# Kernel tuning notes

Measured on AMD Instinct MI355X. Metric: run time of the kernel, lower is better.

The kernel has to match this reference:

```python
import jax, jax.numpy as jnp
import numpy as np

N = 100000
E = 1600000
IN_DIM, HID, OUT = 128, 64, 32
SLOPE = 0.1


def setup_inputs() -> dict:
    key = jax.random.key(0)
    ks = jax.random.split(key, 8)
    x = jax.random.normal(ks[0], (N, IN_DIM), dtype=jnp.float32)
    edge_index = jax.random.randint(ks[1], (2, E), 0, N, dtype=jnp.int64)
    s1 = 1.0 / np.sqrt(IN_DIM)
    s2 = 1.0 / np.sqrt(HID)
    W_l1 = jax.random.uniform(ks[2], (IN_DIM, HID), jnp.float32, -s1, s1)
    W_r1 = jax.random.uniform(ks[3], (IN_DIM, HID), jnp.float32, -s1, s1)
    b1 = jax.random.uniform(ks[4], (HID,), jnp.float32, -s1, s1)
    W_l2 = jax.random.uniform(ks[5], (HID, OUT), jnp.float32, -s2, s2)
    W_r2 = jax.random.uniform(ks[6], (HID, OUT), jnp.float32, -s2, s2)
    b2 = jax.random.uniform(ks[7], (OUT,), jnp.float32, -s2, s2)
    return {"x": x, "edge_index": edge_index,
            "W_l1": W_l1, "W_r1": W_r1, "b1": b1,
            "W_l2": W_l2, "W_r2": W_r2, "b2": b2}


def _sage_conv(h, src, dst, deg_inv, W_l, W_r, b):
    # mean-aggregate neighbor features: gather from src, scatter-add to dst
    agg = jax.ops.segment_sum(h[src], dst, num_segments=N) * deg_inv  # [N, d]
    return agg @ W_l + h @ W_r + b


def reference(x, edge_index, W_l1, W_r1, b1, W_l2, W_r2, b2):
    src, dst = edge_index[0], edge_index[1]
    deg = jax.ops.segment_sum(jnp.ones((E,), x.dtype), dst, num_segments=N)
    deg_inv = (1.0 / jnp.maximum(deg, 1.0))[:, None]  # [N, 1]
    h = jax.nn.leaky_relu(_sage_conv(x, src, dst, deg_inv, W_l1, W_r1, b1), SLOPE)
    z = jax.nn.leaky_relu(_sage_conv(h, src, dst, deg_inv, W_l2, W_r2, b2), SLOPE)
    return z
```

## Files before the change

### kernel.cpp

```cpp
#include <hip/hip_runtime.h>


constexpr int IN_DIM  = 128;
constexpr int HID     = 64;
constexpr int OUT_DIM = 32;
constexpr float SLOPE = 0.1f;
constexpr int NPB_SHIFT = 8;
constexpr int NBMAX = 512;
constexpr int CHUNK = 4096;

typedef unsigned int uint32;
typedef unsigned short ushort16;

__device__ inline float blo(uint32 u) { return __uint_as_float(u << 16); }
__device__ inline float bhi(uint32 u) { return __uint_as_float(u & 0xffff0000u); }
__device__ inline ushort16 f2b(float f) {
    uint32 u = __float_as_uint(f);
    u += 0x7fffu + ((u >> 16) & 1u);
    return (ushort16)(u >> 16);
}
__device__ inline uint32 pack2(float lo, float hi) {
    return (uint32)f2b(lo) | ((uint32)f2b(hi) << 16);
}
__device__ inline void addup(float* acc, uint4 u) {
    acc[0] += blo(u.x); acc[1] += bhi(u.x);
    acc[2] += blo(u.y); acc[3] += bhi(u.y);
    acc[4] += blo(u.z); acc[5] += bhi(u.z);
    acc[6] += blo(u.w); acc[7] += bhi(u.w);
}

__global__ __launch_bounds__(256) void bucket_hist_kernel(
    const int* __restrict__ dst, int* __restrict__ bhist, int E) {
    __shared__ int bh[NBMAX];
    for (int i = threadIdx.x; i < NBMAX; i += 256) bh[i] = 0;
    __syncthreads();
    for (int e = blockIdx.x * 256 + threadIdx.x; e < E; e += gridDim.x * 256)
        atomicAdd(&bh[dst[e] >> NPB_SHIFT], 1);
    __syncthreads();
    for (int b = threadIdx.x; b < NBMAX; b += 256)
        if (bh[b]) atomicAdd(&bhist[b], bh[b]);
}

__global__ __launch_bounds__(512) void bucket_scan_kernel(
    const int* __restrict__ bhist, int* __restrict__ ebase,
    int* __restrict__ pbase, int* __restrict__ bcur,
    int* __restrict__ rowptr, int NB, int N, int E) {
    __shared__ int s1[512], s2[512];
    const int t = threadIdx.x;
    int bh = (t < NB) ? bhist[t] : 0;
    int pd = (bh + 15) & ~15;
    s1[t] = bh; s2[t] = pd; __syncthreads();
    for (int off = 1; off < 512; off <<= 1) {
        int a = (t >= off) ? s1[t - off] : 0;
        int b = (t >= off) ? s2[t - off] : 0;
        __syncthreads();
        s1[t] += a; s2[t] += b;
        __syncthreads();
    }
    ebase[t] = s1[t] - bh;
    pbase[t] = s2[t] - pd;
    bcur[t]  = s2[t] - pd;
    if (t == 0) rowptr[N] = E;
}

__global__ __launch_bounds__(256) void partition_kernel(
    const int* __restrict__ src, const int* __restrict__ dst,
    int* __restrict__ bcur, uint32* __restrict__ pairs, int E, int NB) {
    __shared__ int hist[NBMAX], loff[NBMAX], cur[NBMAX];
    __shared__ int s[256];
    __shared__ uint32 stage[CHUNK];
    const int tid = threadIdx.x;
    const int e0  = blockIdx.x * CHUNK;
    const int cnt = min(CHUNK, E - e0);
    for (int i = tid; i < NBMAX; i += 256) hist[i] = 0;
    __syncthreads();
    int sreg[16], dreg[16];
#pragma unroll
    for (int k = 0; k < 16; ++k) {
        int i = tid + k * 256;
        if (i < cnt) {
            sreg[k] = src[e0 + i];
            dreg[k] = dst[e0 + i];
            atomicAdd(&hist[dreg[k] >> NPB_SHIFT], 1);
        }
    }
    __syncthreads();
    int a0 = hist[2 * tid], a1 = hist[2 * tid + 1];
    s[tid] = a0 + a1; __syncthreads();
    for (int off = 1; off < 256; off <<= 1) {
        int t = (tid >= off) ? s[tid - off] : 0;
        __syncthreads();
        s[tid] += t;
        __syncthreads();
    }
    int ex = s[tid] - (a0 + a1);
    loff[2 * tid] = ex;      loff[2 * tid + 1] = ex + a0;
    cur[2 * tid]  = ex;      cur[2 * tid + 1]  = ex + a0;
    __syncthreads();
#pragma unroll
    for (int k = 0; k < 16; ++k) {
        int i = tid + k * 256;
        if (i < cnt) {
            int b = dreg[k] >> NPB_SHIFT;
            int pos = atomicAdd(&cur[b], 1);
            stage[pos] = (uint32)sreg[k] | ((uint32)(dreg[k] & 255) << 24);
        }
    }
    __syncthreads();
    for (int b = tid; b < NB; b += 256) {
        int cb = hist[b];
        if (cb) {
            int g  = atomicAdd(&bcur[b], cb);
            int lb = loff[b];
            for (int k = 0; k < cb; ++k) pairs[g + k] = stage[lb + k];
        }
    }
}

__global__ __launch_bounds__(256) void fine_bin_kernel(
    const uint32* __restrict__ pairs, const int* __restrict__ bhist,
    const int* __restrict__ ebase, const int* __restrict__ pbase,
    int* __restrict__ rowptr, int* __restrict__ srcs, int N) {
    __shared__ int h2[256], cur[256], s[256];
    const int tid  = threadIdx.x;
    const int b    = blockIdx.x;
    const int n0   = b << NPB_SHIFT;
    const int base = pbase[b];
    const int sz   = bhist[b];
    h2[tid] = 0;
    __syncthreads();
    for (int i = tid; i < sz; i += 256)
        atomicAdd(&h2[pairs[base + i] >> 24], 1);
    __syncthreads();
    int v = h2[tid]; s[tid] = v; __syncthreads();
    for (int off = 1; off < 256; off <<= 1) {
        int t = (tid >= off) ? s[tid - off] : 0;
        __syncthreads();
        s[tid] += t;
        __syncthreads();
    }
    int rp = ebase[b] + s[tid] - v;
    int n  = n0 + tid;
    if (n < N) rowptr[n] = rp;
    cur[tid] = rp;
    __syncthreads();
    for (int i = tid; i < sz; i += 256) {
        uint32 u = pairs[base + i];
        int p = atomicAdd(&cur[u >> 24], 1);
        srcs[p] = (int)(u & 0xFFFFFFu);
    }
}

__global__ __launch_bounds__(256) void gemm1_mfma_kernel(
    const float* __restrict__ x, const float* __restrict__ Wl,
    const float* __restrict__ Wr, const float* __restrict__ b1,
    ushort16* __restrict__ xl, float* __restrict__ xr, int N) {
    using frag = __attribute__((ext_vector_type(8))) short;
    using f32x4 = __attribute__((ext_vector_type(4))) float;
    constexpr int LDA = IN_DIM + 8;
    __shared__ ushort16 Ash[64][LDA];
    __shared__ ushort16 Bsh[128][LDA];
    const int tid = threadIdx.x;
    const int n0  = blockIdx.x * 64;
    {
        const int c = tid & 63;
        for (int k = tid >> 6; k < IN_DIM; k += 4) {
            Bsh[c][k]      = f2b(Wl[k * HID + c]);
            Bsh[c + 64][k] = f2b(Wr[k * HID + c]);
        }
    }
    {
        const int lc  = (tid & 31) * 4;
        for (int row = tid >> 5; row < 64; row += 8) {
            int node = n0 + row;
            float4 xv = (node < N)
                ? *reinterpret_cast<const float4*>(&x[(long)node * IN_DIM + lc])
                : float4{0.f, 0.f, 0.f, 0.f};
            ushort16 pk[4] = {f2b(xv.x), f2b(xv.y), f2b(xv.z), f2b(xv.w)};
            *reinterpret_cast<ushort2*>(&Ash[row][lc])     = ushort2{pk[0], pk[1]};
            *reinterpret_cast<ushort2*>(&Ash[row][lc + 2]) = ushort2{pk[2], pk[3]};
        }
    }
    __syncthreads();
    const int lane = tid & 63;
    const int m0   = (tid >> 6) * 16;
    const int mlo  = lane & 15;
    const int qk   = lane >> 4;
    frag Af[4];
#pragma unroll
    for (int kc = 0; kc < 4; ++kc)
        Af[kc] = *reinterpret_cast<const frag*>(&Ash[m0 + mlo][kc * 32 + qk * 8]);
#pragma unroll
    for (int ct = 0; ct < 8; ++ct) {
        f32x4 acc = {0.f, 0.f, 0.f, 0.f};
#pragma unroll
        for (int kc = 0; kc < 4; ++kc) {
            frag Bf = *reinterpret_cast<const frag*>(&Bsh[ct * 16 + mlo][kc * 32 + qk * 8]);
            acc = __builtin_amdgcn_mfma_f32_16x16x32_bf16(Af[kc], Bf, acc, 0, 0, 0);
        }
        const int col = ct * 16 + mlo;
#pragma unroll
        for (int r = 0; r < 4; ++r) {
            int node = n0 + m0 + qk * 4 + r;
            if (node < N) {
                if (col < HID) xl[(long)node * HID + col] = f2b(acc[r]);
                else           xr[(long)node * HID + (col - HID)] = acc[r] + b1[col - HID];
            }
        }
    }
}

__global__ __launch_bounds__(256) void agg1_kernel(
    const int* __restrict__ rowptr, const int* __restrict__ srcs,
    const uint4* __restrict__ xlq,
    const float* __restrict__ xr,
    uint4* __restrict__ hq, int N) {
    const int lane  = threadIdx.x & 63;
    const int li    = lane & 7;
    const int gbase = lane & 56;
    const int wave  = (blockIdx.x << 2) + (threadIdx.x >> 6);
    const int n     = wave * 8 + (lane >> 3);
    if (n >= N) return;
    const int rp = rowptr[n];
    const int d  = rowptr[n + 1] - rp;
    float acc[8] = {};
    int j = 0;
    while (j + 16 <= d) {
        int sA = srcs[rp + j + li];
        int sB = srcs[rp + j + 8 + li];
        uint4 u0[8], u1[8];
#pragma unroll
        for (int t = 0; t < 8; ++t) {
            int s = __shfl(sA, gbase + t);
            u0[t] = xlq[(long)s * 8 + li];
        }
#pragma unroll
        for (int t = 0; t < 8; ++t) {
            int s = __shfl(sB, gbase + t);
            u1[t] = xlq[(long)s * 8 + li];
        }
#pragma unroll
        for (int t = 0; t < 8; ++t) { addup(acc, u0[t]); addup(acc, u1[t]); }
        j += 16;
    }
    if (j + 8 <= d) {
        int sA = srcs[rp + j + li];
        uint4 u0[8];
#pragma unroll
        for (int t = 0; t < 8; ++t) {
            int s = __shfl(sA, gbase + t);
            u0[t] = xlq[(long)s * 8 + li];
        }
#pragma unroll
        for (int t = 0; t < 8; ++t) addup(acc, u0[t]);
        j += 8;
    }
    int r = d - j;
    if (r > 0) {
        int sA = srcs[rp + j + ((li < r) ? li : 0)];
#pragma unroll
        for (int t = 0; t < 7; ++t) {
            if (t < r) {
                int s = __shfl(sA, gbase + t);
                uint4 u = xlq[(long)s * 8 + li];
                addup(acc, u);
            }
        }
    }
    const float dinv = (d > 0) ? (1.f / (float)d) : 1.f;
    float4 xrA = *reinterpret_cast<const float4*>(&xr[(long)n * HID + 8 * li]);
    float4 xrB = *reinterpret_cast<const float4*>(&xr[(long)n * HID + 8 * li + 4]);
    float h[8];
    h[0] = fmaf(acc[0], dinv, xrA.x); h[1] = fmaf(acc[1], dinv, xrA.y);
    h[2] = fmaf(acc[2], dinv, xrA.z); h[3] = fmaf(acc[3], dinv, xrA.w);
    h[4] = fmaf(acc[4], dinv, xrB.x); h[5] = fmaf(acc[5], dinv, xrB.y);
    h[6] = fmaf(acc[6], dinv, xrB.z); h[7] = fmaf(acc[7], dinv, xrB.w);
#pragma unroll
    for (int t = 0; t < 8; ++t) h[t] = (h[t] > 0.f) ? h[t] : SLOPE * h[t];
    uint4 pk;
    pk.x = pack2(h[0], h[1]); pk.y = pack2(h[2], h[3]);
    pk.z = pack2(h[4], h[5]); pk.w = pack2(h[6], h[7]);
    hq[(long)n * 8 + li] = pk;
}

__global__ __launch_bounds__(256) void gemm2_mfma_kernel(
    const ushort16* __restrict__ hs, const float* __restrict__ Wl2,
    const float* __restrict__ Wr2, const float* __restrict__ b2,
    ushort16* __restrict__ hl, float* __restrict__ hr, int N) {
    using frag = __attribute__((ext_vector_type(8))) short;
    using f32x4 = __attribute__((ext_vector_type(4))) float;
    __shared__ ushort16 Bsh[64][72];
    const int tid = threadIdx.x;
    const int n0  = blockIdx.x * 64;
    {
        const int c = tid & 63;
        for (int k = tid >> 6; k < HID; k += 4) {
            float w = (c < OUT_DIM) ? Wl2[k * OUT_DIM + c]
                                    : Wr2[k * OUT_DIM + (c - OUT_DIM)];
            Bsh[c][k] = f2b(w);
        }
    }
    __syncthreads();
    const int lane = tid & 63;
    const int m0   = (tid >> 6) * 16;
    const int mlo  = lane & 15;
    const int qk   = lane >> 4;
    const int row  = n0 + m0 + mlo;
    const int arow = (row < N) ? row : 0;
    frag Af[2];
#pragma unroll
    for (int kc = 0; kc < 2; ++kc)
        Af[kc] = *reinterpret_cast<const frag*>(&hs[(long)arow * HID + kc * 32 + qk * 8]);
#pragma unroll
    for (int ct = 0; ct < 4; ++ct) {
        f32x4 acc = {0.f, 0.f, 0.f, 0.f};
#pragma unroll
        for (int kc = 0; kc < 2; ++kc) {
            frag Bf = *reinterpret_cast<const frag*>(&Bsh[ct * 16 + mlo][kc * 32 + qk * 8]);
            acc = __builtin_amdgcn_mfma_f32_16x16x32_bf16(Af[kc], Bf, acc, 0, 0, 0);
        }
        const int col = ct * 16 + mlo;
#pragma unroll
        for (int r = 0; r < 4; ++r) {
            int node = n0 + m0 + qk * 4 + r;
            if (node < N) {
                if (col < OUT_DIM) hl[(long)node * OUT_DIM + col] = f2b(acc[r]);
                else hr[(long)node * OUT_DIM + (col - OUT_DIM)] = acc[r] + b2[col - OUT_DIM];
            }
        }
    }
}

__global__ __launch_bounds__(256) void agg2_final_kernel(
    const int* __restrict__ rowptr, const int* __restrict__ srcs,
    const uint4* __restrict__ hlq,
    const float* __restrict__ hr,
    float* __restrict__ z, int N) {
    const int lane  = threadIdx.x & 63;
    const int li    = lane & 3;
    const int gbase = lane & 60;
    const int wave  = (blockIdx.x << 2) + (threadIdx.x >> 6);
    const int n     = wave * 16 + (lane >> 2);
    if (n >= N) return;
    const int rp = rowptr[n];
    const int d  = rowptr[n + 1] - rp;
    float acc[8] = {};
    int j = 0;
    while (j + 16 <= d) {
        int sA = srcs[rp + j + li];
        int sB = srcs[rp + j + 4 + li];
        int sC = srcs[rp + j + 8 + li];
        int sD = srcs[rp + j + 12 + li];
        uint4 u[16];
#pragma unroll
        for (int t = 0; t < 4; ++t) u[t]      = hlq[(long)__shfl(sA, gbase + t) * 4 + li];
#pragma unroll
        for (int t = 0; t < 4; ++t) u[4 + t]  = hlq[(long)__shfl(sB, gbase + t) * 4 + li];
#pragma unroll
        for (int t = 0; t < 4; ++t) u[8 + t]  = hlq[(long)__shfl(sC, gbase + t) * 4 + li];
#pragma unroll
        for (int t = 0; t < 4; ++t) u[12 + t] = hlq[(long)__shfl(sD, gbase + t) * 4 + li];
#pragma unroll
        for (int t = 0; t < 16; ++t) addup(acc, u[t]);
        j += 16;
    }
    while (j + 4 <= d) {
        int sA = srcs[rp + j + li];
        uint4 u[4];
#pragma unroll
        for (int t = 0; t < 4; ++t) u[t] = hlq[(long)__shfl(sA, gbase + t) * 4 + li];
#pragma unroll
        for (int t = 0; t < 4; ++t) addup(acc, u[t]);
        j += 4;
    }
    int r = d - j;
    if (r > 0) {
        int sA = srcs[rp + j + ((li < r) ? li : 0)];
#pragma unroll
        for (int t = 0; t < 3; ++t) {
            if (t < r) {
                uint4 u = hlq[(long)__shfl(sA, gbase + t) * 4 + li];
                addup(acc, u);
            }
        }
    }
    const float dinv = (d > 0) ? (1.f / (float)d) : 1.f;
    float4 hA = *reinterpret_cast<const float4*>(&hr[(long)n * OUT_DIM + 8 * li]);
    float4 hB = *reinterpret_cast<const float4*>(&hr[(long)n * OUT_DIM + 8 * li + 4]);
    float4 vA, vB;
    vA.x = fmaf(acc[0], dinv, hA.x); vA.y = fmaf(acc[1], dinv, hA.y);
    vA.z = fmaf(acc[2], dinv, hA.z); vA.w = fmaf(acc[3], dinv, hA.w);
    vB.x = fmaf(acc[4], dinv, hB.x); vB.y = fmaf(acc[5], dinv, hB.y);
    vB.z = fmaf(acc[6], dinv, hB.z); vB.w = fmaf(acc[7], dinv, hB.w);
    vA.x = (vA.x > 0.f) ? vA.x : SLOPE * vA.x;
    vA.y = (vA.y > 0.f) ? vA.y : SLOPE * vA.y;
    vA.z = (vA.z > 0.f) ? vA.z : SLOPE * vA.z;
    vA.w = (vA.w > 0.f) ? vA.w : SLOPE * vA.w;
    vB.x = (vB.x > 0.f) ? vB.x : SLOPE * vB.x;
    vB.y = (vB.y > 0.f) ? vB.y : SLOPE * vB.y;
    vB.z = (vB.z > 0.f) ? vB.z : SLOPE * vB.z;
    vB.w = (vB.w > 0.f) ? vB.w : SLOPE * vB.w;
    *reinterpret_cast<float4*>(&z[(long)n * OUT_DIM + 8 * li]) = vA;
    *reinterpret_cast<float4*>(&z[(long)n * OUT_DIM + 8 * li + 4]) = vB;
}

extern "C" void kernel_launch(void* const* d_in, const int* in_sizes, int n_in,
                              void* d_out, int out_size, void* d_ws, size_t ws_size,
                              hipStream_t stream) {
    const float* x   = (const float*)d_in[0];
    const int*   ei  = (const int*)d_in[1];
    const float* Wl1 = (const float*)d_in[2];
    const float* Wr1 = (const float*)d_in[3];
    const float* b1  = (const float*)d_in[4];
    const float* Wl2 = (const float*)d_in[5];
    const float* Wr2 = (const float*)d_in[6];
    const float* b2  = (const float*)d_in[7];

    const int N = in_sizes[0] / IN_DIM;
    const int E = in_sizes[1] / 2;
    const int* src = ei;
    const int* dst = ei + E;
    const int NB = (N + 255) >> NPB_SHIFT;

    char* p = (char*)d_ws;
    int* bhist    = (int*)p;           p += sizeof(int) * NBMAX;
    int* ebase    = (int*)p;           p += sizeof(int) * NBMAX;
    int* pbase    = (int*)p;           p += sizeof(int) * NBMAX;
    int* bcur     = (int*)p;           p += sizeof(int) * NBMAX;
    int* rowptr   = (int*)p;           p += sizeof(int) * (N + 4);
    uint32* pairs = (uint32*)p;        p += sizeof(uint32) * ((size_t)E + 16 * NBMAX);
    int* srcs     = (int*)p;           p += sizeof(int) * E;
    ushort16* xl  = (ushort16*)p;      p += sizeof(ushort16) * (size_t)N * HID;
    float* xr     = (float*)p;         p += sizeof(float) * (size_t)N * HID;
    ushort16* h   = (ushort16*)p;      p += sizeof(ushort16) * (size_t)N * HID;
    ushort16* hl  = (ushort16*)p;      p += sizeof(ushort16) * (size_t)N * OUT_DIM;
    float* hr     = (float*)p;         p += sizeof(float) * (size_t)N * OUT_DIM;

    hipMemsetAsync(bhist, 0, sizeof(int) * NBMAX, stream);

    bucket_hist_kernel<<<512, 256, 0, stream>>>(dst, bhist, E);
    bucket_scan_kernel<<<1, 512, 0, stream>>>(bhist, ebase, pbase, bcur, rowptr, NB, N, E);
    partition_kernel<<<(E + CHUNK - 1) / CHUNK, 256, 0, stream>>>(src, dst, bcur, pairs, E, NB);
    fine_bin_kernel<<<NB, 256, 0, stream>>>(pairs, bhist, ebase, pbase, rowptr, srcs, N);
    gemm1_mfma_kernel<<<(N + 63) / 64, 256, 0, stream>>>(x, Wl1, Wr1, b1, xl, xr, N);
    agg1_kernel<<<(N + 31) / 32, 256, 0, stream>>>(rowptr, srcs, (const uint4*)xl, xr,
                                                   (uint4*)h, N);
    gemm2_mfma_kernel<<<(N + 63) / 64, 256, 0, stream>>>(h, Wl2, Wr2, b2, hl, hr, N);
    agg2_final_kernel<<<(N + 63) / 64, 256, 0, stream>>>(rowptr, srcs, (const uint4*)hl, hr,
                                                         (float*)d_out, N);
}
```

Before: 279.1 us.

## Fuse CSR fine-binning into layer-1 aggregation and overlap histogram with GEMM1

Pre-converts weights to bf16 once in a prep kernel and drops the memset. Bucket histogramming now runs as extra blocks inside the GEMM1 launch so the two overlap. The fine-bin sort is merged into the layer-1 aggregation: each block sorts half a bucket's sources in LDS, then aggregates from LDS indices and writes rowptr, degree and srcs for layer 2. The partition write-back is also coalesced using a binary search over bucket offsets. This removes launches and global round-trips, at the cost of redundant per-half histogramming, two-node-per-wave passes, and a fixed LDS capacity (SUBCAP) per half-bucket.

```diff
diff --git a/kernel.cpp b/kernel.cpp
--- a/kernel.cpp
+++ b/kernel.cpp
@@ -8,6 +8,8 @@
 constexpr int NPB_SHIFT = 8;
 constexpr int NBMAX = 512;
 constexpr int CHUNK = 4096;
+constexpr int HIST_BLOCKS = 256;
+constexpr int SUBCAP = 4096;
 
 typedef unsigned int uint32;
 typedef unsigned short ushort16;
@@ -22,6 +24,7 @@
 __device__ inline uint32 pack2(float lo, float hi) {
     return (uint32)f2b(lo) | ((uint32)f2b(hi) << 16);
 }
+__device__ inline float lrelu(float v) { return (v > 0.f) ? v : SLOPE * v; }
 __device__ inline void addup(float* acc, uint4 u) {
     acc[0] += blo(u.x); acc[1] += bhi(u.x);
     acc[2] += blo(u.y); acc[3] += bhi(u.y);
@@ -29,148 +32,50 @@
     acc[6] += blo(u.w); acc[7] += bhi(u.w);
 }
 
-__global__ __launch_bounds__(256) void bucket_hist_kernel(
-    const int* __restrict__ dst, int* __restrict__ bhist, int E) {
-    __shared__ int bh[NBMAX];
-    for (int i = threadIdx.x; i < NBMAX; i += 256) bh[i] = 0;
-    __syncthreads();
-    for (int e = blockIdx.x * 256 + threadIdx.x; e < E; e += gridDim.x * 256)
-        atomicAdd(&bh[dst[e] >> NPB_SHIFT], 1);
-    __syncthreads();
-    for (int b = threadIdx.x; b < NBMAX; b += 256)
-        if (bh[b]) atomicAdd(&bhist[b], bh[b]);
-}
-
-__global__ __launch_bounds__(512) void bucket_scan_kernel(
-    const int* __restrict__ bhist, int* __restrict__ ebase,
-    int* __restrict__ pbase, int* __restrict__ bcur,
-    int* __restrict__ rowptr, int NB, int N, int E) {
-    __shared__ int s1[512], s2[512];
-    const int t = threadIdx.x;
-    int bh = (t < NB) ? bhist[t] : 0;
-    int pd = (bh + 15) & ~15;
-    s1[t] = bh; s2[t] = pd; __syncthreads();
-    for (int off = 1; off < 512; off <<= 1) {
-        int a = (t >= off) ? s1[t - off] : 0;
-        int b = (t >= off) ? s2[t - off] : 0;
-        __syncthreads();
-        s1[t] += a; s2[t] += b;
-        __syncthreads();
-    }
-    ebase[t] = s1[t] - bh;
-    pbase[t] = s2[t] - pd;
-    bcur[t]  = s2[t] - pd;
-    if (t == 0) rowptr[N] = E;
-}
-
-__global__ __launch_bounds__(256) void partition_kernel(
-    const int* __restrict__ src, const int* __restrict__ dst,
-    int* __restrict__ bcur, uint32* __restrict__ pairs, int E, int NB) {
-    __shared__ int hist[NBMAX], loff[NBMAX], cur[NBMAX];
-    __shared__ int s[256];
-    __shared__ uint32 stage[CHUNK];
-    const int tid = threadIdx.x;
-    const int e0  = blockIdx.x * CHUNK;
-    const int cnt = min(CHUNK, E - e0);
-    for (int i = tid; i < NBMAX; i += 256) hist[i] = 0;
-    __syncthreads();
-    int sreg[16], dreg[16];
-#pragma unroll
-    for (int k = 0; k < 16; ++k) {
-        int i = tid + k * 256;
-        if (i < cnt) {
-            sreg[k] = src[e0 + i];
-            dreg[k] = dst[e0 + i];
-            atomicAdd(&hist[dreg[k] >> NPB_SHIFT], 1);
-        }
-    }
-    __syncthreads();
-    int a0 = hist[2 * tid], a1 = hist[2 * tid + 1];
-    s[tid] = a0 + a1; __syncthreads();
-    for (int off = 1; off < 256; off <<= 1) {
-        int t = (tid >= off) ? s[tid - off] : 0;
-        __syncthreads();
-        s[tid] += t;
-        __syncthreads();
-    }
-    int ex = s[tid] - (a0 + a1);
-    loff[2 * tid] = ex;      loff[2 * tid + 1] = ex + a0;
-    cur[2 * tid]  = ex;      cur[2 * tid + 1]  = ex + a0;
-    __syncthreads();
-#pragma unroll
-    for (int k = 0; k < 16; ++k) {
-        int i = tid + k * 256;
-        if (i < cnt) {
-            int b = dreg[k] >> NPB_SHIFT;
-            int pos = atomicAdd(&cur[b], 1);
-            stage[pos] = (uint32)sreg[k] | ((uint32)(dreg[k] & 255) << 24);
-        }
-    }
-    __syncthreads();
-    for (int b = tid; b < NB; b += 256) {
-        int cb = hist[b];
-        if (cb) {
-            int g  = atomicAdd(&bcur[b], cb);
-            int lb = loff[b];
-            for (int k = 0; k < cb; ++k) pairs[g + k] = stage[lb + k];
-        }
-    }
-}
-
-__global__ __launch_bounds__(256) void fine_bin_kernel(
-    const uint32* __restrict__ pairs, const int* __restrict__ bhist,
-    const int* __restrict__ ebase, const int* __restrict__ pbase,
-    int* __restrict__ rowptr, int* __restrict__ srcs, int N) {
-    __shared__ int h2[256], cur[256], s[256];
-    const int tid  = threadIdx.x;
-    const int b    = blockIdx.x;
-    const int n0   = b << NPB_SHIFT;
-    const int base = pbase[b];
-    const int sz   = bhist[b];
-    h2[tid] = 0;
-    __syncthreads();
-    for (int i = tid; i < sz; i += 256)
-        atomicAdd(&h2[pairs[base + i] >> 24], 1);
-    __syncthreads();
-    int v = h2[tid]; s[tid] = v; __syncthreads();
-    for (int off = 1; off < 256; off <<= 1) {
-        int t = (tid >= off) ? s[tid - off] : 0;
-        __syncthreads();
-        s[tid] += t;
-        __syncthreads();
-    }
-    int rp = ebase[b] + s[tid] - v;
-    int n  = n0 + tid;
-    if (n < N) rowptr[n] = rp;
-    cur[tid] = rp;
-    __syncthreads();
-    for (int i = tid; i < sz; i += 256) {
-        uint32 u = pairs[base + i];
-        int p = atomicAdd(&cur[u >> 24], 1);
-        srcs[p] = (int)(u & 0xFFFFFFu);
-    }
-}
-
-__global__ __launch_bounds__(256) void gemm1_mfma_kernel(
-    const float* __restrict__ x, const float* __restrict__ Wl,
-    const float* __restrict__ Wr, const float* __restrict__ b1,
-    ushort16* __restrict__ xl, float* __restrict__ xr, int N) {
+__global__ __launch_bounds__(256) void prep_kernel(
+    const float* __restrict__ Wl1, const float* __restrict__ Wr1,
+    const float* __restrict__ Wl2, const float* __restrict__ Wr2,
+    ushort16* __restrict__ Wb1, ushort16* __restrict__ Wb2,
+    int* __restrict__ bhist) {
+    const int gid = blockIdx.x * 256 + threadIdx.x;
+    if (gid < NBMAX) bhist[gid] = 0;
+    for (int i = gid; i < 128 * 128; i += gridDim.x * 256) {
+        int c = i >> 7, k = i & 127;
+        Wb1[i] = f2b((c < HID) ? Wl1[k * HID + c] : Wr1[k * HID + (c - HID)]);
+    }
+    for (int i = gid; i < 64 * 64; i += gridDim.x * 256) {
+        int c = i >> 6, k = i & 63;
+        Wb2[i] = f2b((c < OUT_DIM) ? Wl2[k * OUT_DIM + c]
+                                   : Wr2[k * OUT_DIM + (c - OUT_DIM)]);
+    }
+}
+
+__global__ __launch_bounds__(256) void gemm1_hist_kernel(
+    const float* __restrict__ x, const ushort16* __restrict__ Wb1,
+    const float* __restrict__ b1,
+    const int* __restrict__ dst, int* __restrict__ bhist,
+    ushort16* __restrict__ xl, float* __restrict__ xr,
+    int N, int E, int ngemm) {
     using frag = __attribute__((ext_vector_type(8))) short;
     using f32x4 = __attribute__((ext_vector_type(4))) float;
     constexpr int LDA = IN_DIM + 8;
     __shared__ ushort16 Ash[64][LDA];
-    __shared__ ushort16 Bsh[128][LDA];
     const int tid = threadIdx.x;
-    const int n0  = blockIdx.x * 64;
+    if (blockIdx.x >= ngemm) {
+        int* bh = (int*)Ash;
+        for (int i = tid; i < NBMAX; i += 256) bh[i] = 0;
+        __syncthreads();
+        const int b0 = blockIdx.x - ngemm;
+        for (int e = b0 * 256 + tid; e < E; e += HIST_BLOCKS * 256)
+            atomicAdd(&bh[dst[e] >> NPB_SHIFT], 1);
+        __syncthreads();
+        for (int b = tid; b < NBMAX; b += 256)
+            if (bh[b]) atomicAdd(&bhist[b], bh[b]);
+        return;
+    }
+    const int n0 = blockIdx.x * 64;
     {
-        const int c = tid & 63;
-        for (int k = tid >> 6; k < IN_DIM; k += 4) {
-            Bsh[c][k]      = f2b(Wl[k * HID + c]);
-            Bsh[c + 64][k] = f2b(Wr[k * HID + c]);
-        }
-    }
-    {
-        const int lc  = (tid & 31) * 4;
+        const int lc = (tid & 31) * 4;
         for (int row = tid >> 5; row < 64; row += 8) {
             int node = n0 + row;
             float4 xv = (node < N)
@@ -195,7 +100,8 @@
         f32x4 acc = {0.f, 0.f, 0.f, 0.f};
 #pragma unroll
         for (int kc = 0; kc < 4; ++kc) {
-            frag Bf = *reinterpret_cast<const frag*>(&Bsh[ct * 16 + mlo][kc * 32 + qk * 8]);
+            frag Bf = *reinterpret_cast<const frag*>(
+                &Wb1[(ct * 16 + mlo) * 128 + kc * 32 + qk * 8]);
             acc = __builtin_amdgcn_mfma_f32_16x16x32_bf16(Af[kc], Bf, acc, 0, 0, 0);
         }
         const int col = ct * 16 + mlo;
@@ -210,97 +116,199 @@
     }
 }
 
-__global__ __launch_bounds__(256) void agg1_kernel(
-    const int* __restrict__ rowptr, const int* __restrict__ srcs,
-    const uint4* __restrict__ xlq,
-    const float* __restrict__ xr,
+__global__ __launch_bounds__(512) void bucket_scan_kernel(
+    const int* __restrict__ bhist, int* __restrict__ pbase,
+    int* __restrict__ bcur, int NB) {
+    __shared__ int s2[512];
+    const int t = threadIdx.x;
+    int bh = (t < NB) ? bhist[t] : 0;
+    int pd = (bh + 15) & ~15;
+    s2[t] = pd; __syncthreads();
+    for (int off = 1; off < 512; off <<= 1) {
+        int b = (t >= off) ? s2[t - off] : 0;
+        __syncthreads();
+        s2[t] += b;
+        __syncthreads();
+    }
+    pbase[t] = s2[t] - pd;
+    bcur[t]  = s2[t] - pd;
+}
+
+__global__ __launch_bounds__(256) void partition_kernel(
+    const int* __restrict__ src, const int* __restrict__ dst,
+    int* __restrict__ bcur, uint32* __restrict__ pairs, int E, int NB) {
+    __shared__ int hist[NBMAX], loff[NBMAX], cur[NBMAX], gbase[NBMAX];
+    __shared__ int s[256];
+    __shared__ uint32 stage[CHUNK];
+    const int tid = threadIdx.x;
+    const int e0  = blockIdx.x * CHUNK;
+    const int cnt = min(CHUNK, E - e0);
+    for (int i = tid; i < NBMAX; i += 256) hist[i] = 0;
+    __syncthreads();
+    int sreg[16], dreg[16];
+#pragma unroll
+    for (int k = 0; k < 16; ++k) {
+        int i = tid + k * 256;
+        if (i < cnt) {
+            sreg[k] = src[e0 + i];
+            dreg[k] = dst[e0 + i];
+            atomicAdd(&hist[dreg[k] >> NPB_SHIFT], 1);
+        }
+    }
+    __syncthreads();
+    int a0 = hist[2 * tid], a1 = hist[2 * tid + 1];
+    s[tid] = a0 + a1; __syncthreads();
+    for (int off = 1; off < 256; off <<= 1) {
+        int t = (tid >= off) ? s[tid - off] : 0;
+        __syncthreads();
+        s[tid] += t;
+        __syncthreads();
+    }
+    int ex = s[tid] - (a0 + a1);
+    loff[2 * tid] = ex;      loff[2 * tid + 1] = ex + a0;
+    cur[2 * tid]  = ex;      cur[2 * tid + 1]  = ex + a0;
+    __syncthreads();
+#pragma unroll
+    for (int k = 0; k < 16; ++k) {
+        int i = tid + k * 256;
+        if (i < cnt) {
+            int b = dreg[k] >> NPB_SHIFT;
+            int pos = atomicAdd(&cur[b], 1);
+            stage[pos] = (uint32)sreg[k] | ((uint32)(dreg[k] & 255) << 24);
+        }
+    }
+    __syncthreads();
+    for (int b = tid; b < NB; b += 256) {
+        int cb = hist[b];
+        if (cb) gbase[b] = atomicAdd(&bcur[b], cb);
+    }
+    __syncthreads();
+    for (int i = tid; i < cnt; i += 256) {
+        int lo = 0, hi = NB - 1;
+        while (lo < hi) {
+            int mid = (lo + hi + 1) >> 1;
+            if (loff[mid] <= i) lo = mid; else hi = mid - 1;
+        }
+        pairs[gbase[lo] + (i - loff[lo])] = stage[i];
+    }
+}
+
+__global__ __launch_bounds__(512) void agg1_sort_kernel(
+    const uint32* __restrict__ pairs, const int* __restrict__ bhist,
+    const int* __restrict__ pbase,
+    const uint4* __restrict__ xlq, const float* __restrict__ xr,
+    uint32* __restrict__ srcs, int* __restrict__ rowptr, int* __restrict__ degA,
     uint4* __restrict__ hq, int N) {
-    const int lane  = threadIdx.x & 63;
-    const int li    = lane & 7;
-    const int gbase = lane & 56;
-    const int wave  = (blockIdx.x << 2) + (threadIdx.x >> 6);
-    const int n     = wave * 8 + (lane >> 3);
-    if (n >= N) return;
-    const int rp = rowptr[n];
-    const int d  = rowptr[n + 1] - rp;
-    float acc[8] = {};
-    int j = 0;
-    while (j + 16 <= d) {
-        int sA = srcs[rp + j + li];
-        int sB = srcs[rp + j + 8 + li];
-        uint4 u0[8], u1[8];
-#pragma unroll
-        for (int t = 0; t < 8; ++t) {
-            int s = __shfl(sA, gbase + t);
-            u0[t] = xlq[(long)s * 8 + li];
-        }
-#pragma unroll
-        for (int t = 0; t < 8; ++t) {
-            int s = __shfl(sB, gbase + t);
-            u1[t] = xlq[(long)s * 8 + li];
-        }
-#pragma unroll
-        for (int t = 0; t < 8; ++t) { addup(acc, u0[t]); addup(acc, u1[t]); }
-        j += 16;
-    }
-    if (j + 8 <= d) {
-        int sA = srcs[rp + j + li];
-        uint4 u0[8];
-#pragma unroll
-        for (int t = 0; t < 8; ++t) {
-            int s = __shfl(sA, gbase + t);
-            u0[t] = xlq[(long)s * 8 + li];
-        }
-#pragma unroll
-        for (int t = 0; t < 8; ++t) addup(acc, u0[t]);
-        j += 8;
-    }
-    int r = d - j;
-    if (r > 0) {
-        int sA = srcs[rp + j + ((li < r) ? li : 0)];
-#pragma unroll
-        for (int t = 0; t < 7; ++t) {
-            if (t < r) {
-                int s = __shfl(sA, gbase + t);
-                uint4 u = xlq[(long)s * 8 + li];
-                addup(acc, u);
-            }
-        }
-    }
-    const float dinv = (d > 0) ? (1.f / (float)d) : 1.f;
-    float4 xrA = *reinterpret_cast<const float4*>(&xr[(long)n * HID + 8 * li]);
-    float4 xrB = *reinterpret_cast<const float4*>(&xr[(long)n * HID + 8 * li + 4]);
-    float h[8];
-    h[0] = fmaf(acc[0], dinv, xrA.x); h[1] = fmaf(acc[1], dinv, xrA.y);
-    h[2] = fmaf(acc[2], dinv, xrA.z); h[3] = fmaf(acc[3], dinv, xrA.w);
-    h[4] = fmaf(acc[4], dinv, xrB.x); h[5] = fmaf(acc[5], dinv, xrB.y);
-    h[6] = fmaf(acc[6], dinv, xrB.z); h[7] = fmaf(acc[7], dinv, xrB.w);
-#pragma unroll
-    for (int t = 0; t < 8; ++t) h[t] = (h[t] > 0.f) ? h[t] : SLOPE * h[t];
-    uint4 pk;
-    pk.x = pack2(h[0], h[1]); pk.y = pack2(h[2], h[3]);
-    pk.z = pack2(h[4], h[5]); pk.w = pack2(h[6], h[7]);
-    hq[(long)n * 8 + li] = pk;
+    __shared__ int hist[256], loff[256], cur[128];
+    __shared__ int lsrc[SUBCAP];
+    const int tid  = threadIdx.x;
+    const int bkt  = blockIdx.x >> 1;
+    const int half = blockIdx.x & 1;
+    const int n0   = bkt << NPB_SHIFT;
+    const int base = pbase[bkt];
+    const int sz   = bhist[bkt];
+    if (tid < 256) hist[tid] = 0;
+    __syncthreads();
+    for (int i = tid; i < sz; i += 512)
+        atomicAdd(&hist[pairs[base + i] >> 24], 1);
+    __syncthreads();
+    int v = (tid < 256) ? hist[tid] : 0;
+    if (tid < 256) loff[tid] = v;
+    __syncthreads();
+    for (int off = 1; off < 256; off <<= 1) {
+        int t = (tid >= off && tid < 256) ? loff[tid - off] : 0;
+        __syncthreads();
+        if (tid < 256) loff[tid] += t;
+        __syncthreads();
+    }
+    if (tid < 256) loff[tid] -= v;
+    __syncthreads();
+    if (half == 0 && tid < 256 && n0 + tid < N) {
+        rowptr[n0 + tid] = base + loff[tid];
+        degA[n0 + tid]   = hist[tid];
+    }
+    const int hbase = loff[half << 7];
+    const int hcnt  = (half ? sz : loff[128]) - hbase;
+    if (tid < 128) cur[tid] = loff[(half << 7) + tid] - hbase;
+    __syncthreads();
+    for (int i = tid; i < sz; i += 512) {
+        uint32 u = pairs[base + i];
+        int dl = u >> 24;
+        if ((dl >> 7) == half) {
+            int pos = atomicAdd(&cur[dl & 127], 1);
+            lsrc[pos] = (int)(u & 0xFFFFFFu);
+        }
+    }
+    __syncthreads();
+    for (int i = tid; i < hcnt; i += 512)
+        srcs[base + hbase + i] = (uint32)lsrc[i];
+    const int lane = tid & 63;
+    const int wid  = tid >> 6;
+    const int li   = lane & 7;
+#pragma unroll
+    for (int pass = 0; pass < 2; ++pass) {
+        const int nl = (half << 7) + pass * 64 + wid * 8 + (lane >> 3);
+        const int n  = n0 + nl;
+        if (n >= N) continue;
+        const int lo0 = loff[nl] - hbase;
+        const int d   = hist[nl];
+        float acc[8] = {};
+        int j = 0;
+        while (j + 16 <= d) {
+            int i0[8], i1[8];
+#pragma unroll
+            for (int t = 0; t < 8; ++t) i0[t] = lsrc[lo0 + j + t];
+#pragma unroll
+            for (int t = 0; t < 8; ++t) i1[t] = lsrc[lo0 + j + 8 + t];
+            uint4 u0[8], u1[8];
+#pragma unroll
+            for (int t = 0; t < 8; ++t) u0[t] = xlq[(long)i0[t] * 8 + li];
+#pragma unroll
+            for (int t = 0; t < 8; ++t) u1[t] = xlq[(long)i1[t] * 8 + li];
+#pragma unroll
+            for (int t = 0; t < 8; ++t) { addup(acc, u0[t]); addup(acc, u1[t]); }
+            j += 16;
+        }
+        if (j + 8 <= d) {
+            int i0[8];
+#pragma unroll
+            for (int t = 0; t < 8; ++t) i0[t] = lsrc[lo0 + j + t];
+            uint4 u0[8];
+#pragma unroll
+            for (int t = 0; t < 8; ++t) u0[t] = xlq[(long)i0[t] * 8 + li];
+#pragma unroll
+            for (int t = 0; t < 8; ++t) addup(acc, u0[t]);
+            j += 8;
+        }
+        for (; j < d; ++j) {
+            uint4 u = xlq[(long)lsrc[lo0 + j] * 8 + li];
+            addup(acc, u);
+        }
+        const float dinv = (d > 0) ? (1.f / (float)d) : 1.f;
+        float4 xrA = *reinterpret_cast<const float4*>(&xr[(long)n * HID + 8 * li]);
+        float4 xrB = *reinterpret_cast<const float4*>(&xr[(long)n * HID + 8 * li + 4]);
+        float h[8];
+        h[0] = fmaf(acc[0], dinv, xrA.x); h[1] = fmaf(acc[1], dinv, xrA.y);
+        h[2] = fmaf(acc[2], dinv, xrA.z); h[3] = fmaf(acc[3], dinv, xrA.w);
+        h[4] = fmaf(acc[4], dinv, xrB.x); h[5] = fmaf(acc[5], dinv, xrB.y);
+        h[6] = fmaf(acc[6], dinv, xrB.z); h[7] = fmaf(acc[7], dinv, xrB.w);
+#pragma unroll
+        for (int t = 0; t < 8; ++t) h[t] = lrelu(h[t]);
+        uint4 pk;
+        pk.x = pack2(h[0], h[1]); pk.y = pack2(h[2], h[3]);
+        pk.z = pack2(h[4], h[5]); pk.w = pack2(h[6], h[7]);
+        hq[(long)n * 8 + li] = pk;
+    }
 }
 
 __global__ __launch_bounds__(256) void gemm2_mfma_kernel(
-    const ushort16* __restrict__ hs, const float* __restrict__ Wl2,
-    const float* __restrict__ Wr2, const float* __restrict__ b2,
+    const ushort16* __restrict__ hs, const ushort16* __restrict__ Wb2,
+    const float* __restrict__ b2,
     ushort16* __restrict__ hl, float* __restrict__ hr, int N) {
     using frag = __attribute__((ext_vector_type(8))) short;
     using f32x4 = __attribute__((ext_vector_type(4))) float;
-    __shared__ ushort16 Bsh[64][72];
-    const int tid = threadIdx.x;
-    const int n0  = blockIdx.x * 64;
-    {
-        const int c = tid & 63;
-        for (int k = tid >> 6; k < HID; k += 4) {
-            float w = (c < OUT_DIM) ? Wl2[k * OUT_DIM + c]
-                                    : Wr2[k * OUT_DIM + (c - OUT_DIM)];
-            Bsh[c][k] = f2b(w);
-        }
-    }
-    __syncthreads();
+    const int tid  = threadIdx.x;
+    const int n0   = blockIdx.x * 64;
     const int lane = tid & 63;
     const int m0   = (tid >> 6) * 16;
     const int mlo  = lane & 15;
@@ -316,7 +324,8 @@
         f32x4 acc = {0.f, 0.f, 0.f, 0.f};
 #pragma unroll
         for (int kc = 0; kc < 2; ++kc) {
-            frag Bf = *reinterpret_cast<const frag*>(&Bsh[ct * 16 + mlo][kc * 32 + qk * 8]);
+            frag Bf = *reinterpret_cast<const frag*>(
+                &Wb2[(ct * 16 + mlo) * 64 + kc * 32 + qk * 8]);
             acc = __builtin_amdgcn_mfma_f32_16x16x32_bf16(Af[kc], Bf, acc, 0, 0, 0);
         }
         const int col = ct * 16 + mlo;
@@ -332,9 +341,9 @@
 }
 
 __global__ __launch_bounds__(256) void agg2_final_kernel(
-    const int* __restrict__ rowptr, const int* __restrict__ srcs,
-    const uint4* __restrict__ hlq,
-    const float* __restrict__ hr,
+    const int* __restrict__ rowptr, const int* __restrict__ degA,
+    const uint32* __restrict__ srcs,
+    const uint4* __restrict__ hlq, const float* __restrict__ hr,
     float* __restrict__ z, int N) {
     const int lane  = threadIdx.x & 63;
     const int li    = lane & 3;
@@ -343,14 +352,14 @@
     const int n     = wave * 16 + (lane >> 2);
     if (n >= N) return;
     const int rp = rowptr[n];
-    const int d  = rowptr[n + 1] - rp;
+    const int d  = degA[n];
     float acc[8] = {};
     int j = 0;
     while (j + 16 <= d) {
-        int sA = srcs[rp + j + li];
-        int sB = srcs[rp + j + 4 + li];
-        int sC = srcs[rp + j + 8 + li];
-        int sD = srcs[rp + j + 12 + li];
+        int sA = (int)srcs[rp + j + li];
+        int sB = (int)srcs[rp + j + 4 + li];
+        int sC = (int)srcs[rp + j + 8 + li];
+        int sD = (int)srcs[rp + j + 12 + li];
         uint4 u[16];
 #pragma unroll
         for (int t = 0; t < 4; ++t) u[t]      = hlq[(long)__shfl(sA, gbase + t) * 4 + li];
@@ -365,7 +374,7 @@
         j += 16;
     }
     while (j + 4 <= d) {
-        int sA = srcs[rp + j + li];
+        int sA = (int)srcs[rp + j + li];
         uint4 u[4];
 #pragma unroll
         for (int t = 0; t < 4; ++t) u[t] = hlq[(long)__shfl(sA, gbase + t) * 4 + li];
@@ -375,7 +384,7 @@
     }
     int r = d - j;
     if (r > 0) {
-        int sA = srcs[rp + j + ((li < r) ? li : 0)];
+        int sA = (int)srcs[rp + j + ((li < r) ? li : 0)];
 #pragma unroll
         for (int t = 0; t < 3; ++t) {
             if (t < r) {
@@ -388,18 +397,10 @@
     float4 hA = *reinterpret_cast<const float4*>(&hr[(long)n * OUT_DIM + 8 * li]);
     float4 hB = *reinterpret_cast<const float4*>(&hr[(long)n * OUT_DIM + 8 * li + 4]);
     float4 vA, vB;
-    vA.x = fmaf(acc[0], dinv, hA.x); vA.y = fmaf(acc[1], dinv, hA.y);
-    vA.z = fmaf(acc[2], dinv, hA.z); vA.w = fmaf(acc[3], dinv, hA.w);
-    vB.x = fmaf(acc[4], dinv, hB.x); vB.y = fmaf(acc[5], dinv, hB.y);
-    vB.z = fmaf(acc[6], dinv, hB.z); vB.w = fmaf(acc[7], dinv, hB.w);
-    vA.x = (vA.x > 0.f) ? vA.x : SLOPE * vA.x;
-    vA.y = (vA.y > 0.f) ? vA.y : SLOPE * vA.y;
-    vA.z = (vA.z > 0.f) ? vA.z : SLOPE * vA.z;
-    vA.w = (vA.w > 0.f) ? vA.w : SLOPE * vA.w;
-    vB.x = (vB.x > 0.f) ? vB.x : SLOPE * vB.x;
-    vB.y = (vB.y > 0.f) ? vB.y : SLOPE * vB.y;
-    vB.z = (vB.z > 0.f) ? vB.z : SLOPE * vB.z;
-    vB.w = (vB.w > 0.f) ? vB.w : SLOPE * vB.w;
+    vA.x = lrelu(fmaf(acc[0], dinv, hA.x)); vA.y = lrelu(fmaf(acc[1], dinv, hA.y));
+    vA.z = lrelu(fmaf(acc[2], dinv, hA.z)); vA.w = lrelu(fmaf(acc[3], dinv, hA.w));
+    vB.x = lrelu(fmaf(acc[4], dinv, hB.x)); vB.y = lrelu(fmaf(acc[5], dinv, hB.y));
+    vB.z = lrelu(fmaf(acc[6], dinv, hB.z)); vB.w = lrelu(fmaf(acc[7], dinv, hB.w));
     *reinterpret_cast<float4*>(&z[(long)n * OUT_DIM + 8 * li]) = vA;
     *reinterpret_cast<float4*>(&z[(long)n * OUT_DIM + 8 * li + 4]) = vB;
 }
@@ -424,28 +425,31 @@
 
     char* p = (char*)d_ws;
     int* bhist    = (int*)p;           p += sizeof(int) * NBMAX;
-    int* ebase    = (int*)p;           p += sizeof(int) * NBMAX;
     int* pbase    = (int*)p;           p += sizeof(int) * NBMAX;
     int* bcur     = (int*)p;           p += sizeof(int) * NBMAX;
     int* rowptr   = (int*)p;           p += sizeof(int) * (N + 4);
+    int* degA     = (int*)p;           p += sizeof(int) * (N + 4);
     uint32* pairs = (uint32*)p;        p += sizeof(uint32) * ((size_t)E + 16 * NBMAX);
-    int* srcs     = (int*)p;           p += sizeof(int) * E;
+    uint32* srcs  = (uint32*)p;        p += sizeof(uint32) * ((size_t)E + 16 * NBMAX);
+    ushort16* Wb1 = (ushort16*)p;      p += sizeof(ushort16) * 128 * 128;
+    ushort16* Wb2 = (ushort16*)p;      p += sizeof(ushort16) * 64 * 64;
     ushort16* xl  = (ushort16*)p;      p += sizeof(ushort16) * (size_t)N * HID;
     float* xr     = (float*)p;         p += sizeof(float) * (size_t)N * HID;
     ushort16* h   = (ushort16*)p;      p += sizeof(ushort16) * (size_t)N * HID;
     ushort16* hl  = (ushort16*)p;      p += sizeof(ushort16) * (size_t)N * OUT_DIM;
     float* hr     = (float*)p;         p += sizeof(float) * (size_t)N * OUT_DIM;
 
-    hipMemsetAsync(bhist, 0, sizeof(int) * NBMAX, stream);
-
-    bucket_hist_kernel<<<512, 256, 0, stream>>>(dst, bhist, E);
-    bucket_scan_kernel<<<1, 512, 0, stream>>>(bhist, ebase, pbase, bcur, rowptr, NB, N, E);
+    const int ngemm = (N + 63) / 64;
+    prep_kernel<<<32, 256, 0, stream>>>(Wl1, Wr1, Wl2, Wr2, Wb1, Wb2, bhist);
+    gemm1_hist_kernel<<<ngemm + HIST_BLOCKS, 256, 0, stream>>>(
+        x, Wb1, b1, dst, bhist, xl, xr, N, E, ngemm);
+    bucket_scan_kernel<<<1, 512, 0, stream>>>(bhist, pbase, bcur, NB);
     partition_kernel<<<(E + CHUNK - 1) / CHUNK, 256, 0, stream>>>(src, dst, bcur, pairs, E, NB);
-    fine_bin_kernel<<<NB, 256, 0, stream>>>(pairs, bhist, ebase, pbase, rowptr, srcs, N);
-    gemm1_mfma_kernel<<<(N + 63) / 64, 256, 0, stream>>>(x, Wl1, Wr1, b1, xl, xr, N);
-    agg1_kernel<<<(N + 31) / 32, 256, 0, stream>>>(rowptr, srcs, (const uint4*)xl, xr,
-                                                   (uint4*)h, N);
-    gemm2_mfma_kernel<<<(N + 63) / 64, 256, 0, stream>>>(h, Wl2, Wr2, b2, hl, hr, N);
-    agg2_final_kernel<<<(N + 63) / 64, 256, 0, stream>>>(rowptr, srcs, (const uint4*)hl, hr,
+    agg1_sort_kernel<<<NB * 2, 512, 0, stream>>>(pairs, bhist, pbase,
+                                                 (const uint4*)xl, xr,
+                                                 srcs, rowptr, degA, (uint4*)h, N);
+    gemm2_mfma_kernel<<<(N + 63) / 64, 256, 0, stream>>>(h, Wb2, b2, hl, hr, N);
+    agg2_final_kernel<<<(N + 63) / 64, 256, 0, stream>>>(rowptr, degA, srcs,
+                                                         (const uint4*)hl, hr,
                                                          (float*)d_out, N);
 }
```

New measurement: 274.2 us. Within noise of the previous version (-1.8%).
